# Kernel tuning notes

Hardware: AMD Instinct MI355X
Metric: run time of the kernel (lower is better)

Reference implementation:

```python
import jax, jax.numpy as jnp
import numpy as np

NUM_CLASSES = 4
NUM_PROTOTYPE = 8
D = 512
N = 200704  # 16 * 112 * 112 flattened tokens
GAMMA = 0.999        # EMA momentum (self.gamma)
EPS_SINK = 0.05      # sinkhorn epsilon
SINK_ITERS = 3       # sinkhorn iterations


def l2_normalize(x, axis=-1, eps=1e-12):
    n = jnp.linalg.norm(x, axis=axis, keepdims=True)
    return x / jnp.maximum(n, eps)


def layer_norm(x, g, b, eps=1e-5):
    mu = jnp.mean(x, axis=-1, keepdims=True)
    var = jnp.var(x, axis=-1, keepdims=True)
    return (x - mu) / jnp.sqrt(var + eps) * g + b


def masked_sinkhorn(scores, sel):
    # scores: [N, M] similarity to this class's prototypes; sel: [N] bool row mask
    # Faithful masked re-expression of distributed_sinkhorn (which gathers rows
    # where gt_seg == k); zeroed rows contribute nothing to any normalization.
    M = scores.shape[1]
    self32 = sel.astype(scores.dtype)[:, None]
    L = jnp.exp(scores / EPS_SINK) * self32           # [N, M]
    B = jnp.maximum(sel.sum(), 1).astype(scores.dtype)  # number of selected rows
    L = L / jnp.maximum(L.sum(), 1e-30)

    def body(L, _):
        col = L.sum(axis=0, keepdims=True)            # per-prototype mass
        L = L / jnp.maximum(col, 1e-30) / M
        row = L.sum(axis=1, keepdims=True)            # per-token mass
        L = (L / jnp.maximum(row, 1e-30) / B) * self32
        return L, None

    L, _ = jax.lax.scan(body, L, None, length=SINK_ITERS)
    L = L * B
    idx = jnp.argmax(L, axis=1)
    # hard one-hot assignment (deterministic stand-in for hard gumbel_softmax)
    q = jax.nn.one_hot(idx, M, dtype=scores.dtype) * self32
    return q


def prototype_learning(_c, pred, gt_seg, masks, protos, momentum):
    # _c [N, D], pred/gt_seg [N], masks [N, M, K], protos [K, M, D]
    correct = gt_seg == pred
    new_rows = []
    for k in range(NUM_CLASSES):  # small fixed class loop, as in the original
        sel = gt_seg == k
        q = masked_sinkhorn(masks[:, :, k], sel)      # [N, M]
        m_k = (correct & sel).astype(_c.dtype)        # [N]
        m_q = q * m_k[:, None]                        # masked assignments
        c_q = _c * m_k[:, None]                       # masked features
        f = m_q.T @ c_q                               # [M, D] aggregation
        n = m_q.sum(axis=0)                           # [M] per-prototype counts
        f = l2_normalize(f)
        upd = momentum * protos[k] + (1.0 - momentum) * f
        valid = (n != 0) & (sel.sum() > 0) & (n.sum() > 0)
        new_rows.append(jnp.where(valid[:, None], upd, protos[k]))
    return l2_normalize(jnp.stack(new_rows, axis=0))


def reference(feats, ln_gamma, ln_beta, mask_gamma, mask_beta, prototypes, gt_seg):
    _c = l2_normalize(layer_norm(feats, ln_gamma, ln_beta))       # [N, D]
    protos = l2_normalize(prototypes)                             # [K, M, D]
    masks = jnp.einsum('nd,kmd->nmk', _c, protos)                 # [N, M, K]
    out_seg = layer_norm(jnp.max(masks, axis=1), mask_gamma, mask_beta)  # [N, K]
    pred = jnp.argmax(out_seg, axis=1)
    new_protos = prototype_learning(_c, pred, gt_seg.astype(jnp.int32), masks, protos, GAMMA)
    return out_seg, new_protos


def setup_inputs() -> dict:
    key = jax.random.key(0)
    k1, k2, k3 = jax.random.split(key, 3)
    return {
        'feats': jax.random.normal(k1, (N, D), dtype=jnp.float32),
        'ln_gamma': jnp.ones((D,), jnp.float32),
        'ln_beta': jnp.zeros((D,), jnp.float32),
        'mask_gamma': jnp.ones((NUM_CLASSES,), jnp.float32),
        'mask_beta': jnp.zeros((NUM_CLASSES,), jnp.float32),
        'prototypes': 0.02 * jax.random.normal(k2, (NUM_CLASSES, NUM_PROTOTYPE, D), dtype=jnp.float32),
        'gt_seg': jax.random.randint(k3, (N,), 0, NUM_CLASSES, dtype=jnp.int32),
    }
```

## Files before the change

kernel.cpp:

```cpp
#include <hip/hip_runtime.h>
#include <math.h>

#define NROWS 200704
#define DIM 512
#define NKM 32

#define OFF_RED0   0
#define OFF_RED1   32
#define OFF_RED2   64
#define OFF_CNT    96
#define OFF_NP     100
#define OFF_CUR    192
#define OFF_BASE   2240
#define OFF_FACC   2304
#define ZERO_FLOATS 18688
#define OFF_SUMGP  18688
#define OFF_BP     18720
#define OFF_SCAL   18752
#define OFF_G2GB   18816
#define OFF_PROTON 19840
#define OFF_GPT    36224
#define OFF_RSTATS 52608
#define OFF_E      855424
#define OFF_FLAGS  2461056
#define OFF_SORT   2661760

__device__ __forceinline__ float block_reduce_sum(float v, float* sm) {
    int t = threadIdx.x;
    sm[t] = v; __syncthreads();
    #pragma unroll
    for (int o = 128; o > 0; o >>= 1) {
        if (t < o) sm[t] += sm[t + o];
        __syncthreads();
    }
    float r = sm[0]; __syncthreads();
    return r;
}

__global__ __launch_bounds__(256) void k_prep(const float* __restrict__ protos,
                                              const float* __restrict__ g,
                                              const float* __restrict__ b,
                                              float* __restrict__ ws) {
    __shared__ float sm[256];
    int t = threadIdx.x, j = blockIdx.x;
    if (j < NKM) {
        const float* p = protos + j * DIM;
        float v = p[t] * p[t] + p[t + 256] * p[t + 256];
        float ss = block_reduce_sum(v, sm);
        float den = fmaxf(sqrtf(ss), 1e-12f);
        float sgp = 0.f, sbp = 0.f;
        for (int d = t; d < DIM; d += 256) {
            float pn = p[d] / den;
            ws[OFF_PROTON + j * DIM + d] = pn;
            float gp = g[d] * pn;
            ws[OFF_GPT + j * DIM + d] = gp;
            sgp += gp; sbp += b[d] * pn;
        }
        float s1 = block_reduce_sum(sgp, sm);
        float s2 = block_reduce_sum(sbp, sm);
        if (t == 0) { ws[OFF_SUMGP + j] = s1; ws[OFF_BP + j] = s2; }
    } else {
        float a = 0.f, c = 0.f, e = 0.f;
        for (int d = t; d < DIM; d += 256) {
            float gv = g[d], bv = b[d];
            ws[OFF_G2GB + 2 * d]     = gv * gv;
            ws[OFF_G2GB + 2 * d + 1] = gv * bv;
            a += gv * gv; c += gv * bv; e += bv * bv;
        }
        float s1 = block_reduce_sum(a, sm);
        float s2 = block_reduce_sum(c, sm);
        float s3 = block_reduce_sum(e, sm);
        if (t == 0) { ws[OFF_SCAL] = s1; ws[OFF_SCAL + 1] = s2; ws[OFF_SCAL + 2] = s3; }
    }
}

#define STATS(XR, r) { \
    float _a = XR.x, _b = XR.y, _c = XR.z, _d = XR.w; \
    sx[r] += _a + _b + _c + _d; \
    float _a2 = _a * _a, _b2 = _b * _b, _c2 = _c * _c, _d2 = _d * _d; \
    sxx[r] += _a2 + _b2 + _c2 + _d2; \
    sxg2[r]  = fmaf(_a, gA.x, fmaf(_b, gA.z, fmaf(_c, gB.x, fmaf(_d, gB.z, sxg2[r])))); \
    sx2g2[r] = fmaf(_a2, gA.x, fmaf(_b2, gA.z, fmaf(_c2, gB.x, fmaf(_d2, gB.z, sx2g2[r])))); \
    sxgb[r]  = fmaf(_a, gA.y, fmaf(_b, gA.w, fmaf(_c, gB.y, fmaf(_d, gB.w, sxgb[r])))); \
}

#define EPILOGUE(DJ, r) { \
    float a_sx = sx[r], a_sxx = sxx[r], a_sxg2 = sxg2[r], a_sx2g2 = sx2g2[r], a_sxgb = sxgb[r]; \
    _Pragma("unroll") \
    for (int m = 1; m <= 4; m <<= 1) { \
        a_sx += __shfl_xor(a_sx, m, 64); \
        a_sxx += __shfl_xor(a_sxx, m, 64); \
        a_sxg2 += __shfl_xor(a_sxg2, m, 64); \
        a_sx2g2 += __shfl_xor(a_sx2g2, m, 64); \
        a_sxgb += __shfl_xor(a_sxgb, m, 64); \
        _Pragma("unroll") \
        for (int j = 0; j < NKM; ++j) DJ[j] += __shfl_xor(DJ[j], m, 64); \
    } \
    float mu = a_sx * (1.0f / DIM); \
    float var = a_sxx * (1.0f / DIM) - mu * mu; \
    float istd = 1.0f / sqrtf(var + 1e-5f); \
    float l2 = istd * istd * (a_sx2g2 - 2.0f * mu * a_sxg2 + mu * mu * s_scal[0]) \
             + 2.0f * istd * (a_sxgb - mu * s_scal[1]) + s_scal[2]; \
    float L = sqrtf(fmaxf(l2, 0.0f)); \
    float invL = 1.0f / fmaxf(L, 1e-12f); \
    float aa = istd * invL; \
    _Pragma("unroll") \
    for (int j = 0; j < NKM; ++j) DJ[j] = aa * (DJ[j] - mu * s_sumgp[j]) + invL * s_bp[j]; \
    float om[4]; \
    _Pragma("unroll") \
    for (int k = 0; k < 4; ++k) { \
        float m0 = DJ[k * 8]; \
        _Pragma("unroll") \
        for (int m = 1; m < 8; ++m) m0 = fmaxf(m0, DJ[k * 8 + m]); \
        om[k] = m0; \
    } \
    float mu4 = 0.25f * (om[0] + om[1] + om[2] + om[3]); \
    float e0 = om[0] - mu4, e1 = om[1] - mu4, e2 = om[2] - mu4, e3 = om[3] - mu4; \
    float v4 = 0.25f * (e0 * e0 + e1 * e1 + e2 * e2 + e3 * e3); \
    float is4 = 1.0f / sqrtf(v4 + 1e-5f); \
    float o0 = e0 * is4 * mg[0] + mb[0]; \
    float o1 = e1 * is4 * mg[1] + mb[1]; \
    float o2 = e2 * is4 * mg[2] + mb[2]; \
    float o3 = e3 * is4 * mg[3] + mb[3]; \
    int pred = 0; float bo = o0; \
    if (o1 > bo) { bo = o1; pred = 1; } \
    if (o2 > bo) { bo = o2; pred = 2; } \
    if (o3 > bo) { bo = o3; pred = 3; } \
    int row = row0 + r; \
    int gtv = gt_seg[row] & 3; \
    if (li == 0) { \
        *(float4*)(out + (size_t)row * 4) = make_float4(o0, o1, o2, o3); \
        ((int*)ws)[OFF_FLAGS + row] = gtv | ((pred == gtv) ? 4 : 0); \
        *(float4*)(ws + OFF_RSTATS + (size_t)row * 4) = make_float4(mu, istd, invL, 0.f); \
        float ev[8]; \
        _Pragma("unroll") \
        for (int m = 0; m < 8; ++m) { \
            float s = DJ[m]; \
            s = (gtv == 1) ? DJ[8 + m]  : s; \
            s = (gtv == 2) ? DJ[16 + m] : s; \
            s = (gtv == 3) ? DJ[24 + m] : s; \
            ev[m] = expf(s * 20.0f); \
        } \
        *(float4*)(ws + OFF_E + (size_t)row * 8)     = make_float4(ev[0], ev[1], ev[2], ev[3]); \
        *(float4*)(ws + OFF_E + (size_t)row * 8 + 4) = make_float4(ev[4], ev[5], ev[6], ev[7]); \
    } \
}

__global__ __launch_bounds__(256, 2) void k_main(const float* __restrict__ feats,
                                                 const float* __restrict__ mg,
                                                 const float* __restrict__ mb,
                                                 const int* __restrict__ gt_seg,
                                                 float* __restrict__ ws,
                                                 float* __restrict__ out) {
    __shared__ float gpt[NKM * DIM];
    __shared__ float s_sumgp[NKM], s_bp[NKM], s_scal[3];
    int t = threadIdx.x;
    {
        const float4* s4 = (const float4*)(ws + OFF_GPT);
        float4* d4 = (float4*)gpt;
        #pragma unroll 4
        for (int i = t; i < NKM * DIM / 4; i += 256) d4[i] = s4[i];
        if (t < NKM) { s_sumgp[t] = ws[OFF_SUMGP + t]; s_bp[t] = ws[OFF_BP + t]; }
        if (t < 3) s_scal[t] = ws[OFF_SCAL + t];
    }
    __syncthreads();
    int lane = t & 63, wv = t >> 6;
    int oct = lane >> 3, li = lane & 7;
    int row0 = blockIdx.x * 128 + wv * 32 + oct * 4;
    const float* xb = feats + (size_t)row0 * DIM;

    float dj0[NKM], dj1[NKM], dj2[NKM], dj3[NKM];
    #pragma unroll
    for (int j = 0; j < NKM; ++j) { dj0[j] = 0.f; dj1[j] = 0.f; dj2[j] = 0.f; dj3[j] = 0.f; }
    float sx[4] = {0,0,0,0}, sxx[4] = {0,0,0,0}, sxg2[4] = {0,0,0,0};
    float sx2g2[4] = {0,0,0,0}, sxgb[4] = {0,0,0,0};

    for (int c = 0; c < 16; ++c) {
        int d0 = c * 32 + li * 4;
        float4 x0 = *(const float4*)(xb + d0);
        float4 x1 = *(const float4*)(xb + DIM + d0);
        float4 x2 = *(const float4*)(xb + 2 * DIM + d0);
        float4 x3 = *(const float4*)(xb + 3 * DIM + d0);
        float4 gA = *(const float4*)(ws + OFF_G2GB + 2 * d0);
        float4 gB = *(const float4*)(ws + OFF_G2GB + 2 * d0 + 4);
        STATS(x0, 0) STATS(x1, 1) STATS(x2, 2) STATS(x3, 3)
        #pragma unroll
        for (int j = 0; j < NKM; ++j) {
            float4 w = *(const float4*)(gpt + j * DIM + d0);
            dj0[j] = fmaf(x0.x, w.x, fmaf(x0.y, w.y, fmaf(x0.z, w.z, fmaf(x0.w, w.w, dj0[j]))));
            dj1[j] = fmaf(x1.x, w.x, fmaf(x1.y, w.y, fmaf(x1.z, w.z, fmaf(x1.w, w.w, dj1[j]))));
            dj2[j] = fmaf(x2.x, w.x, fmaf(x2.y, w.y, fmaf(x2.z, w.z, fmaf(x2.w, w.w, dj2[j]))));
            dj3[j] = fmaf(x3.x, w.x, fmaf(x3.y, w.y, fmaf(x3.z, w.z, fmaf(x3.w, w.w, dj3[j]))));
        }
    }
    EPILOGUE(dj0, 0)
    EPILOGUE(dj1, 1)
    EPILOGUE(dj2, 2)
    EPILOGUE(dj3, 3)
}

__global__ __launch_bounds__(256) void k_red0(const int* __restrict__ gt_seg,
                                              float* __restrict__ ws) {
    __shared__ float lred[NKM];
    __shared__ int lcnt[4];
    int t = threadIdx.x;
    if (t < NKM) lred[t] = 0.f;
    if (t < 4) lcnt[t] = 0;
    __syncthreads();
    int row = blockIdx.x * 256 + t;
    int gt = gt_seg[row] & 3;
    float4 ea = *(const float4*)(ws + OFF_E + (size_t)row * 8);
    float4 eb = *(const float4*)(ws + OFF_E + (size_t)row * 8 + 4);
    atomicAdd(&lred[gt * 8 + 0], ea.x); atomicAdd(&lred[gt * 8 + 1], ea.y);
    atomicAdd(&lred[gt * 8 + 2], ea.z); atomicAdd(&lred[gt * 8 + 3], ea.w);
    atomicAdd(&lred[gt * 8 + 4], eb.x); atomicAdd(&lred[gt * 8 + 5], eb.y);
    atomicAdd(&lred[gt * 8 + 6], eb.z); atomicAdd(&lred[gt * 8 + 7], eb.w);
    atomicAdd(&lcnt[gt], 1);
    __syncthreads();
    if (t < NKM) atomicAdd(&ws[OFF_RED0 + t], lred[t]);
    if (t < 4) atomicAdd(&((int*)ws)[OFF_CNT + t], lcnt[t]);
}

__global__ __launch_bounds__(256) void k_red1(const int* __restrict__ gt_seg,
                                              float* __restrict__ ws) {
    __shared__ float S0p[4], Bk[4], a1[NKM], lred[NKM];
    int t = threadIdx.x;
    if (t < 4) {
        float s = 0.f;
        #pragma unroll
        for (int m = 0; m < 8; ++m) s += ws[OFF_RED0 + t * 8 + m];
        S0p[t] = fmaxf(s, 1e-30f);
        Bk[t] = fmaxf((float)((const int*)ws)[OFF_CNT + t], 1.0f);
    }
    if (t < NKM) lred[t] = 0.f;
    __syncthreads();
    if (t < NKM) {
        float col = ws[OFF_RED0 + t] / S0p[t >> 3];
        a1[t] = 1.0f / (fmaxf(col, 1e-30f) * 8.0f);
    }
    __syncthreads();
    int row = blockIdx.x * 256 + t;
    int gt = gt_seg[row] & 3;
    float4 ea = *(const float4*)(ws + OFF_E + (size_t)row * 8);
    float4 eb = *(const float4*)(ws + OFF_E + (size_t)row * 8 + 4);
    float ev[8] = {ea.x, ea.y, ea.z, ea.w, eb.x, eb.y, eb.z, eb.w};
    float dotv = 0.f;
    #pragma unroll
    for (int m = 0; m < 8; ++m) dotv += ev[m] * a1[gt * 8 + m];
    float row1 = dotv / S0p[gt];
    float r1 = 1.0f / (fmaxf(row1, 1e-30f) * Bk[gt]);
    #pragma unroll
    for (int m = 0; m < 8; ++m) atomicAdd(&lred[gt * 8 + m], ev[m] * r1);
    __syncthreads();
    if (t < NKM) atomicAdd(&ws[OFF_RED1 + t], lred[t]);
}

__global__ __launch_bounds__(256) void k_red2(const int* __restrict__ gt_seg,
                                              float* __restrict__ ws) {
    __shared__ float S0p[4], Bk[4], a1[NKM], a2[NKM], lred[NKM];
    int t = threadIdx.x;
    if (t < 4) {
        float s = 0.f;
        #pragma unroll
        for (int m = 0; m < 8; ++m) s += ws[OFF_RED0 + t * 8 + m];
        S0p[t] = fmaxf(s, 1e-30f);
        Bk[t] = fmaxf((float)((const int*)ws)[OFF_CNT + t], 1.0f);
    }
    if (t < NKM) lred[t] = 0.f;
    __syncthreads();
    if (t < NKM) {
        float col = ws[OFF_RED0 + t] / S0p[t >> 3];
        a1[t] = 1.0f / (fmaxf(col, 1e-30f) * 8.0f);
    }
    __syncthreads();
    if (t < NKM) {
        float col2 = a1[t] * ws[OFF_RED1 + t] / S0p[t >> 3];
        a2[t] = 1.0f / (fmaxf(col2, 1e-30f) * 8.0f);
    }
    __syncthreads();
    int row = blockIdx.x * 256 + t;
    int gt = gt_seg[row] & 3;
    float4 ea = *(const float4*)(ws + OFF_E + (size_t)row * 8);
    float4 eb = *(const float4*)(ws + OFF_E + (size_t)row * 8 + 4);
    float ev[8] = {ea.x, ea.y, ea.z, ea.w, eb.x, eb.y, eb.z, eb.w};
    float dotv = 0.f;
    #pragma unroll
    for (int m = 0; m < 8; ++m) dotv += ev[m] * a1[gt * 8 + m];
    float row1 = dotv / S0p[gt];
    float r1 = 1.0f / (fmaxf(row1, 1e-30f) * Bk[gt]);
    float dot2 = 0.f;
    #pragma unroll
    for (int m = 0; m < 8; ++m) dot2 += ev[m] * a1[gt * 8 + m] * a2[gt * 8 + m];
    float row2 = dot2 / S0p[gt] * r1;
    float r2 = 1.0f / (fmaxf(row2, 1e-30f) * Bk[gt]);
    #pragma unroll
    for (int m = 0; m < 8; ++m) atomicAdd(&lred[gt * 8 + m], ev[m] * r1 * r2);
    __syncthreads();
    if (t < NKM) atomicAdd(&ws[OFF_RED2 + t], lred[t]);
}

__global__ __launch_bounds__(256) void k_assign(float* __restrict__ ws) {
    __shared__ float S0p[4], Bk[4], a1[NKM], a2[NKM], F[NKM];
    __shared__ int ln[NKM];
    int t = threadIdx.x;
    if (t < 4) {
        float s = 0.f;
        #pragma unroll
        for (int m = 0; m < 8; ++m) s += ws[OFF_RED0 + t * 8 + m];
        S0p[t] = fmaxf(s, 1e-30f);
        Bk[t] = fmaxf((float)((const int*)ws)[OFF_CNT + t], 1.0f);
    }
    if (t < NKM) ln[t] = 0;
    __syncthreads();
    if (t < NKM) {
        float col = ws[OFF_RED0 + t] / S0p[t >> 3];
        a1[t] = 1.0f / (fmaxf(col, 1e-30f) * 8.0f);
    }
    __syncthreads();
    if (t < NKM) {
        float col2 = a1[t] * ws[OFF_RED1 + t] / S0p[t >> 3];
        a2[t] = 1.0f / (fmaxf(col2, 1e-30f) * 8.0f);
    }
    __syncthreads();
    if (t < NKM) {
        float col3 = a1[t] * a2[t] * ws[OFF_RED2 + t] / S0p[t >> 3];
        float a3 = 1.0f / (fmaxf(col3, 1e-30f) * 8.0f);
        F[t] = a1[t] * a2[t] * a3;
    }
    __syncthreads();
    int row = blockIdx.x * 256 + t;
    int flag = ((const int*)ws)[OFF_FLAGS + row];
    int slotv = -1;
    if (flag & 4) {
        int gt = flag & 3;
        float4 ea = *(const float4*)(ws + OFF_E + (size_t)row * 8);
        float4 eb = *(const float4*)(ws + OFF_E + (size_t)row * 8 + 4);
        float ev[8] = {ea.x, ea.y, ea.z, ea.w, eb.x, eb.y, eb.z, eb.w};
        int js = 0; float bv = ev[0] * F[gt * 8];
        #pragma unroll
        for (int m = 1; m < 8; ++m) {
            float v = ev[m] * F[gt * 8 + m];
            if (v > bv) { bv = v; js = m; }
        }
        slotv = gt * 8 + js;
        atomicAdd(&ln[slotv], 1);
    }
    ((int*)ws)[OFF_FLAGS + row] = slotv;
    __syncthreads();
    if (t < NKM && ln[t]) atomicAdd(&((int*)ws)[OFF_NP + t], ln[t]);
}

__global__ void k_prefix(float* __restrict__ ws) {
    if (threadIdx.x == 0) {
        int acc = 0;
        for (int s = 0; s < NKM; ++s) {
            ((int*)ws)[OFF_BASE + s] = acc;
            acc += ((const int*)ws)[OFF_NP + s];
        }
    }
}

__global__ __launch_bounds__(256) void k_scatter(float* __restrict__ ws) {
    int row = blockIdx.x * 256 + threadIdx.x;
    int s = ((const int*)ws)[OFF_FLAGS + row];
    if (s >= 0) {
        int pos = atomicAdd(&((int*)ws)[OFF_CUR + s * 64], 1);
        ((int*)ws)[OFF_SORT + ((const int*)ws)[OFF_BASE + s] + pos] = row;
    }
}

__global__ __launch_bounds__(256) void k_agg(const float* __restrict__ feats,
                                             const float* __restrict__ g,
                                             const float* __restrict__ b,
                                             float* __restrict__ ws) {
    int t = threadIdx.x;
    int slot = blockIdx.x >> 4, ch = blockIdx.x & 15;
    int n = ((const int*)ws)[OFF_NP + slot];
    int base = ((const int*)ws)[OFF_BASE + slot];
    int r0 = base + (ch * n) / 16;
    int r1 = base + ((ch + 1) * n) / 16;
    if (r0 >= r1) return;
    const int* sortl = (const int*)ws + OFF_SORT;
    float2 gv = *(const float2*)(g + 2 * t);
    float2 bv = *(const float2*)(b + 2 * t);
    float acc0 = 0.f, acc1 = 0.f;
    #pragma unroll 4
    for (int i = r0; i < r1; ++i) {
        int row = sortl[i];
        float4 rs = *(const float4*)(ws + OFF_RSTATS + (size_t)row * 4);
        float2 x = *(const float2*)(feats + (size_t)row * DIM + 2 * t);
        acc0 += ((x.x - rs.x) * rs.y * gv.x + bv.x) * rs.z;
        acc1 += ((x.y - rs.x) * rs.y * gv.y + bv.y) * rs.z;
    }
    atomicAdd(&ws[OFF_FACC + slot * DIM + 2 * t],     acc0);
    atomicAdd(&ws[OFF_FACC + slot * DIM + 2 * t + 1], acc1);
}

__global__ __launch_bounds__(256) void k_final(float* __restrict__ ws,
                                               float* __restrict__ out) {
    __shared__ float sm[256];
    int t = threadIdx.x, j = blockIdx.x, k = j >> 3;
    int nj = ((const int*)ws)[OFF_NP + j];
    int ck = ((const int*)ws)[OFF_CNT + k];
    int nsum = 0;
    #pragma unroll
    for (int m = 0; m < 8; ++m) nsum += ((const int*)ws)[OFF_NP + k * 8 + m];
    int d0 = t, d1 = t + 256;
    float f0 = ws[OFF_FACC + j * DIM + d0];
    float f1 = ws[OFF_FACC + j * DIM + d1];
    float nf = block_reduce_sum(f0 * f0 + f1 * f1, sm);
    float fin = 1.0f / fmaxf(sqrtf(nf), 1e-12f);
    float pn0 = ws[OFF_PROTON + j * DIM + d0];
    float pn1 = ws[OFF_PROTON + j * DIM + d1];
    bool valid = (nj != 0) && (ck > 0) && (nsum > 0);
    float r0 = valid ? (0.999f * pn0 + 0.001f * (f0 * fin)) : pn0;
    float r1 = valid ? (0.999f * pn1 + 0.001f * (f1 * fin)) : pn1;
    float n2 = block_reduce_sum(r0 * r0 + r1 * r1, sm);
    float i2 = 1.0f / fmaxf(sqrtf(n2), 1e-12f);
    out[(size_t)NROWS * 4 + j * DIM + d0] = r0 * i2;
    out[(size_t)NROWS * 4 + j * DIM + d1] = r1 * i2;
}

extern "C" void kernel_launch(void* const* d_in, const int* in_sizes, int n_in,
                              void* d_out, int out_size, void* d_ws, size_t ws_size,
                              hipStream_t stream) {
    const float* feats = (const float*)d_in[0];
    const float* ln_g  = (const float*)d_in[1];
    const float* ln_b  = (const float*)d_in[2];
    const float* mg    = (const float*)d_in[3];
    const float* mb    = (const float*)d_in[4];
    const float* prot  = (const float*)d_in[5];
    const int*   gt    = (const int*)d_in[6];
    float* out = (float*)d_out;
    float* ws  = (float*)d_ws;

    hipMemsetAsync(d_ws, 0, ZERO_FLOATS * 4, stream);
    k_prep<<<33, 256, 0, stream>>>(prot, ln_g, ln_b, ws);
    k_main<<<NROWS / 128, 256, 0, stream>>>(feats, mg, mb, gt, ws, out);
    k_red0<<<NROWS / 256, 256, 0, stream>>>(gt, ws);
    k_red1<<<NROWS / 256, 256, 0, stream>>>(gt, ws);
    k_red2<<<NROWS / 256, 256, 0, stream>>>(gt, ws);
    k_assign<<<NROWS / 256, 256, 0, stream>>>(ws);
    k_prefix<<<1, 64, 0, stream>>>(ws);
    k_scatter<<<NROWS / 256, 256, 0, stream>>>(ws);
    k_agg<<<NKM * 16, 256, 0, stream>>>(feats, ln_g, ln_b, ws);
    k_final<<<NKM, 256, 0, stream>>>(ws, out);
}
```

Before: 804.3 us.

## Compute token-prototype similarities with split-bf16 MFMA instead of scalar FP32 FMAs

```diff
diff --git a/kernel.cpp b/kernel.cpp
--- a/kernel.cpp
+++ b/kernel.cpp
@@ -1,4 +1,5 @@
 #include <hip/hip_runtime.h>
+#include <hip/hip_bf16.h>
 #include <math.h>
 
 #define NROWS 200704
@@ -19,11 +20,24 @@
 #define OFF_SCAL   18752
 #define OFF_G2GB   18816
 #define OFF_PROTON 19840
-#define OFF_GPT    36224
-#define OFF_RSTATS 52608
-#define OFF_E      855424
-#define OFF_FLAGS  2461056
-#define OFF_SORT   2661760
+#define OFF_WHI    36224
+#define OFF_WLO    44544
+#define OFF_RSTATS 52864
+#define OFF_E      855680
+#define OFF_FLAGS  2461312
+#define OFF_SORT   2662016
+
+typedef __attribute__((ext_vector_type(8)))  short short8;
+typedef __attribute__((ext_vector_type(16))) float f32x16;
+
+union ABFrag { unsigned int u[4]; short8 s; };
+
+__device__ __forceinline__ unsigned int pk2(float a, float b) {
+    __hip_bfloat162 h2 = __float22bfloat162_rn(make_float2(a, b));
+    union { __hip_bfloat162 h; unsigned int u; } cv;
+    cv.h = h2;
+    return cv.u;
+}
 
 __device__ __forceinline__ float block_reduce_sum(float v, float* sm) {
     int t = threadIdx.x;
@@ -49,12 +63,18 @@
         float ss = block_reduce_sum(v, sm);
         float den = fmaxf(sqrtf(ss), 1e-12f);
         float sgp = 0.f, sbp = 0.f;
+        unsigned short* whi = (unsigned short*)ws + 2 * OFF_WHI + j * 520;
+        unsigned short* wlo = (unsigned short*)ws + 2 * OFF_WLO + j * 520;
         for (int d = t; d < DIM; d += 256) {
             float pn = p[d] / den;
             ws[OFF_PROTON + j * DIM + d] = pn;
-            float gp = g[d] * pn;
-            ws[OFF_GPT + j * DIM + d] = gp;
-            sgp += gp; sbp += b[d] * pn;
+            float w = g[d] * pn;
+            unsigned int hb = pk2(w, 0.f) & 0xffffu;
+            float hf = __uint_as_float(hb << 16);
+            unsigned int lb = pk2(w - hf, 0.f) & 0xffffu;
+            whi[d] = (unsigned short)hb;
+            wlo[d] = (unsigned short)lb;
+            sgp += w; sbp += b[d] * pn;
         }
         float s1 = block_reduce_sum(sgp, sm);
         float s2 = block_reduce_sum(sbp, sm);
@@ -74,77 +94,17 @@
     }
 }
 
-#define STATS(XR, r) { \
-    float _a = XR.x, _b = XR.y, _c = XR.z, _d = XR.w; \
-    sx[r] += _a + _b + _c + _d; \
-    float _a2 = _a * _a, _b2 = _b * _b, _c2 = _c * _c, _d2 = _d * _d; \
-    sxx[r] += _a2 + _b2 + _c2 + _d2; \
-    sxg2[r]  = fmaf(_a, gA.x, fmaf(_b, gA.z, fmaf(_c, gB.x, fmaf(_d, gB.z, sxg2[r])))); \
-    sx2g2[r] = fmaf(_a2, gA.x, fmaf(_b2, gA.z, fmaf(_c2, gB.x, fmaf(_d2, gB.z, sx2g2[r])))); \
-    sxgb[r]  = fmaf(_a, gA.y, fmaf(_b, gA.w, fmaf(_c, gB.y, fmaf(_d, gB.w, sxgb[r])))); \
-}
-
-#define EPILOGUE(DJ, r) { \
-    float a_sx = sx[r], a_sxx = sxx[r], a_sxg2 = sxg2[r], a_sx2g2 = sx2g2[r], a_sxgb = sxgb[r]; \
-    _Pragma("unroll") \
-    for (int m = 1; m <= 4; m <<= 1) { \
-        a_sx += __shfl_xor(a_sx, m, 64); \
-        a_sxx += __shfl_xor(a_sxx, m, 64); \
-        a_sxg2 += __shfl_xor(a_sxg2, m, 64); \
-        a_sx2g2 += __shfl_xor(a_sx2g2, m, 64); \
-        a_sxgb += __shfl_xor(a_sxgb, m, 64); \
-        _Pragma("unroll") \
-        for (int j = 0; j < NKM; ++j) DJ[j] += __shfl_xor(DJ[j], m, 64); \
-    } \
-    float mu = a_sx * (1.0f / DIM); \
-    float var = a_sxx * (1.0f / DIM) - mu * mu; \
-    float istd = 1.0f / sqrtf(var + 1e-5f); \
-    float l2 = istd * istd * (a_sx2g2 - 2.0f * mu * a_sxg2 + mu * mu * s_scal[0]) \
-             + 2.0f * istd * (a_sxgb - mu * s_scal[1]) + s_scal[2]; \
-    float L = sqrtf(fmaxf(l2, 0.0f)); \
-    float invL = 1.0f / fmaxf(L, 1e-12f); \
-    float aa = istd * invL; \
-    _Pragma("unroll") \
-    for (int j = 0; j < NKM; ++j) DJ[j] = aa * (DJ[j] - mu * s_sumgp[j]) + invL * s_bp[j]; \
-    float om[4]; \
-    _Pragma("unroll") \
-    for (int k = 0; k < 4; ++k) { \
-        float m0 = DJ[k * 8]; \
-        _Pragma("unroll") \
-        for (int m = 1; m < 8; ++m) m0 = fmaxf(m0, DJ[k * 8 + m]); \
-        om[k] = m0; \
-    } \
-    float mu4 = 0.25f * (om[0] + om[1] + om[2] + om[3]); \
-    float e0 = om[0] - mu4, e1 = om[1] - mu4, e2 = om[2] - mu4, e3 = om[3] - mu4; \
-    float v4 = 0.25f * (e0 * e0 + e1 * e1 + e2 * e2 + e3 * e3); \
-    float is4 = 1.0f / sqrtf(v4 + 1e-5f); \
-    float o0 = e0 * is4 * mg[0] + mb[0]; \
-    float o1 = e1 * is4 * mg[1] + mb[1]; \
-    float o2 = e2 * is4 * mg[2] + mb[2]; \
-    float o3 = e3 * is4 * mg[3] + mb[3]; \
-    int pred = 0; float bo = o0; \
-    if (o1 > bo) { bo = o1; pred = 1; } \
-    if (o2 > bo) { bo = o2; pred = 2; } \
-    if (o3 > bo) { bo = o3; pred = 3; } \
-    int row = row0 + r; \
-    int gtv = gt_seg[row] & 3; \
-    if (li == 0) { \
-        *(float4*)(out + (size_t)row * 4) = make_float4(o0, o1, o2, o3); \
-        ((int*)ws)[OFF_FLAGS + row] = gtv | ((pred == gtv) ? 4 : 0); \
-        *(float4*)(ws + OFF_RSTATS + (size_t)row * 4) = make_float4(mu, istd, invL, 0.f); \
-        float ev[8]; \
-        _Pragma("unroll") \
-        for (int m = 0; m < 8; ++m) { \
-            float s = DJ[m]; \
-            s = (gtv == 1) ? DJ[8 + m]  : s; \
-            s = (gtv == 2) ? DJ[16 + m] : s; \
-            s = (gtv == 3) ? DJ[24 + m] : s; \
-            ev[m] = expf(s * 20.0f); \
-        } \
-        *(float4*)(ws + OFF_E + (size_t)row * 8)     = make_float4(ev[0], ev[1], ev[2], ev[3]); \
-        *(float4*)(ws + OFF_E + (size_t)row * 8 + 4) = make_float4(ev[4], ev[5], ev[6], ev[7]); \
-    } \
-}
+#define ST1(XV, G2V, GBV) { float _x = (XV); float _x2 = _x * _x; \
+    sx += _x; sxx += _x2; \
+    sxg2  = fmaf(_x,  (G2V), sxg2); \
+    sx2g2 = fmaf(_x2, (G2V), sx2g2); \
+    sxgb  = fmaf(_x,  (GBV), sxgb); }
+
+#define PAIRSPLIT(A0, B0, HO, LO) { \
+    unsigned int _h = pk2((A0), (B0)); HO = _h; \
+    float _ha = __uint_as_float(_h << 16); \
+    float _hb = __uint_as_float(_h & 0xffff0000u); \
+    LO = pk2((A0) - _ha, (B0) - _hb); }
 
 __global__ __launch_bounds__(256, 2) void k_main(const float* __restrict__ feats,
                                                  const float* __restrict__ mg,
@@ -152,51 +112,126 @@
                                                  const int* __restrict__ gt_seg,
                                                  float* __restrict__ ws,
                                                  float* __restrict__ out) {
-    __shared__ float gpt[NKM * DIM];
-    __shared__ float s_sumgp[NKM], s_bp[NKM], s_scal[3];
+    __shared__ __align__(16) unsigned short ls_whi[32 * 520];
+    __shared__ __align__(16) unsigned short ls_wlo[32 * 520];
+    __shared__ __align__(16) float ls_g2gb[1024];
     int t = threadIdx.x;
     {
-        const float4* s4 = (const float4*)(ws + OFF_GPT);
-        float4* d4 = (float4*)gpt;
-        #pragma unroll 4
-        for (int i = t; i < NKM * DIM / 4; i += 256) d4[i] = s4[i];
-        if (t < NKM) { s_sumgp[t] = ws[OFF_SUMGP + t]; s_bp[t] = ws[OFF_BP + t]; }
-        if (t < 3) s_scal[t] = ws[OFF_SCAL + t];
-    }
-    __syncthreads();
-    int lane = t & 63, wv = t >> 6;
-    int oct = lane >> 3, li = lane & 7;
-    int row0 = blockIdx.x * 128 + wv * 32 + oct * 4;
-    const float* xb = feats + (size_t)row0 * DIM;
-
-    float dj0[NKM], dj1[NKM], dj2[NKM], dj3[NKM];
-    #pragma unroll
-    for (int j = 0; j < NKM; ++j) { dj0[j] = 0.f; dj1[j] = 0.f; dj2[j] = 0.f; dj3[j] = 0.f; }
-    float sx[4] = {0,0,0,0}, sxx[4] = {0,0,0,0}, sxg2[4] = {0,0,0,0};
-    float sx2g2[4] = {0,0,0,0}, sxgb[4] = {0,0,0,0};
-
-    for (int c = 0; c < 16; ++c) {
-        int d0 = c * 32 + li * 4;
-        float4 x0 = *(const float4*)(xb + d0);
-        float4 x1 = *(const float4*)(xb + DIM + d0);
-        float4 x2 = *(const float4*)(xb + 2 * DIM + d0);
-        float4 x3 = *(const float4*)(xb + 3 * DIM + d0);
-        float4 gA = *(const float4*)(ws + OFF_G2GB + 2 * d0);
-        float4 gB = *(const float4*)(ws + OFF_G2GB + 2 * d0 + 4);
-        STATS(x0, 0) STATS(x1, 1) STATS(x2, 2) STATS(x3, 3)
-        #pragma unroll
-        for (int j = 0; j < NKM; ++j) {
-            float4 w = *(const float4*)(gpt + j * DIM + d0);
-            dj0[j] = fmaf(x0.x, w.x, fmaf(x0.y, w.y, fmaf(x0.z, w.z, fmaf(x0.w, w.w, dj0[j]))));
-            dj1[j] = fmaf(x1.x, w.x, fmaf(x1.y, w.y, fmaf(x1.z, w.z, fmaf(x1.w, w.w, dj1[j]))));
-            dj2[j] = fmaf(x2.x, w.x, fmaf(x2.y, w.y, fmaf(x2.z, w.z, fmaf(x2.w, w.w, dj2[j]))));
-            dj3[j] = fmaf(x3.x, w.x, fmaf(x3.y, w.y, fmaf(x3.z, w.z, fmaf(x3.w, w.w, dj3[j]))));
-        }
-    }
-    EPILOGUE(dj0, 0)
-    EPILOGUE(dj1, 1)
-    EPILOGUE(dj2, 2)
-    EPILOGUE(dj3, 3)
+        const float4* sh = (const float4*)(ws + OFF_WHI);
+        float4* dh = (float4*)ls_whi;
+        for (int i = t; i < 2080; i += 256) dh[i] = sh[i];
+        const float4* sl = (const float4*)(ws + OFF_WLO);
+        float4* dl = (float4*)ls_wlo;
+        for (int i = t; i < 2080; i += 256) dl[i] = sl[i];
+        const float4* sg = (const float4*)(ws + OFF_G2GB);
+        float4* dg = (float4*)ls_g2gb;
+        dg[t] = sg[t];
+    }
+    __syncthreads();
+
+    int wv = t >> 6, l = t & 63;
+    int h = l >> 5, c32 = l & 31;
+    int row0 = blockIdx.x * 128 + wv * 32;
+    const float* xrow = feats + (size_t)(row0 + c32) * DIM + h * 8;
+    const unsigned short* bhp = ls_whi + c32 * 520 + h * 8;
+    const unsigned short* blp = ls_wlo + c32 * 520 + h * 8;
+    const float4* g4 = ((const float4*)ls_g2gb) + h * 4;
+
+    f32x16 acc;
+    #pragma unroll
+    for (int i = 0; i < 16; ++i) acc[i] = 0.f;
+    float sx = 0.f, sxx = 0.f, sxg2 = 0.f, sx2g2 = 0.f, sxgb = 0.f;
+
+    #pragma unroll 4
+    for (int kc = 0; kc < 32; ++kc) {
+        float4 xa = *(const float4*)(xrow + kc * 16);
+        float4 xb = *(const float4*)(xrow + kc * 16 + 4);
+        float4 ga  = g4[kc * 8 + 0];
+        float4 gb_ = g4[kc * 8 + 1];
+        float4 gc  = g4[kc * 8 + 2];
+        float4 gd  = g4[kc * 8 + 3];
+        ST1(xa.x, ga.x,  ga.y)  ST1(xa.y, ga.z,  ga.w)
+        ST1(xa.z, gb_.x, gb_.y) ST1(xa.w, gb_.z, gb_.w)
+        ST1(xb.x, gc.x,  gc.y)  ST1(xb.y, gc.z,  gc.w)
+        ST1(xb.z, gd.x,  gd.y)  ST1(xb.w, gd.z,  gd.w)
+        ABFrag ah, al;
+        PAIRSPLIT(xa.x, xa.y, ah.u[0], al.u[0])
+        PAIRSPLIT(xa.z, xa.w, ah.u[1], al.u[1])
+        PAIRSPLIT(xb.x, xb.y, ah.u[2], al.u[2])
+        PAIRSPLIT(xb.z, xb.w, ah.u[3], al.u[3])
+        short8 bh = *(const short8*)(bhp + kc * 16);
+        short8 bl = *(const short8*)(blp + kc * 16);
+        acc = __builtin_amdgcn_mfma_f32_32x32x16_bf16(ah.s, bh, acc, 0, 0, 0);
+        acc = __builtin_amdgcn_mfma_f32_32x32x16_bf16(ah.s, bl, acc, 0, 0, 0);
+        acc = __builtin_amdgcn_mfma_f32_32x32x16_bf16(al.s, bh, acc, 0, 0, 0);
+    }
+
+    sx    += __shfl_xor(sx, 32, 64);
+    sxx   += __shfl_xor(sxx, 32, 64);
+    sxg2  += __shfl_xor(sxg2, 32, 64);
+    sx2g2 += __shfl_xor(sx2g2, 32, 64);
+    sxgb  += __shfl_xor(sxgb, 32, 64);
+
+    float scal0 = ws[OFF_SCAL], scal1 = ws[OFF_SCAL + 1], scal2 = ws[OFF_SCAL + 2];
+    float mu  = sx * (1.0f / DIM);
+    float var = sxx * (1.0f / DIM) - mu * mu;
+    float istd = 1.0f / sqrtf(var + 1e-5f);
+    float l2v = istd * istd * (sx2g2 - 2.0f * mu * sxg2 + mu * mu * scal0)
+              + 2.0f * istd * (sxgb - mu * scal1) + scal2;
+    float L = sqrtf(fmaxf(l2v, 0.0f));
+    float invL = 1.0f / fmaxf(L, 1e-12f);
+    float aa = istd * invL;
+    if (l < 32)
+        *(float4*)(ws + OFF_RSTATS + (size_t)(row0 + l) * 4) = make_float4(mu, istd, invL, 0.f);
+
+    float wsum = ws[OFF_SUMGP + c32], wbp = ws[OFF_BP + c32];
+    float mg0 = mg[0], mg1 = mg[1], mg2 = mg[2], mg3 = mg[3];
+    float mb0 = mb[0], mb1 = mb[1], mb2 = mb[2], mb3 = mb[3];
+    int q = c32 >> 3;
+    int li8 = c32 & 7;
+
+    #pragma unroll
+    for (int r = 0; r < 16; ++r) {
+        int rowt = (r & 3) + 8 * (r >> 2) + 4 * h;
+        int grow = row0 + rowt;
+        float mu_r = __shfl(mu, rowt, 64);
+        float aa_r = __shfl(aa, rowt, 64);
+        float il_r = __shfl(invL, rowt, 64);
+        float s = aa_r * (acc[r] - mu_r * wsum) + il_r * wbp;
+        float m = s;
+        m = fmaxf(m, __shfl_xor(m, 1, 64));
+        m = fmaxf(m, __shfl_xor(m, 2, 64));
+        m = fmaxf(m, __shfl_xor(m, 4, 64));
+        float vA = m;
+        float vB = __shfl_xor(vA, 8, 64);
+        float vC = __shfl_xor(vA, 16, 64);
+        float vD = __shfl_xor(vB, 16, 64);
+        float o0 = (q == 0) ? vA : (q == 1) ? vB : (q == 2) ? vC : vD;
+        float o1 = (q == 1) ? vA : (q == 0) ? vB : (q == 3) ? vC : vD;
+        float o2 = (q == 2) ? vA : (q == 3) ? vB : (q == 0) ? vC : vD;
+        float o3 = (q == 3) ? vA : (q == 2) ? vB : (q == 1) ? vC : vD;
+        float mu4 = 0.25f * (o0 + o1 + o2 + o3);
+        float e0 = o0 - mu4, e1 = o1 - mu4, e2 = o2 - mu4, e3 = o3 - mu4;
+        float v4 = 0.25f * (e0 * e0 + e1 * e1 + e2 * e2 + e3 * e3);
+        float is4 = 1.0f / sqrtf(v4 + 1e-5f);
+        float f0 = e0 * is4 * mg0 + mb0;
+        float f1 = e1 * is4 * mg1 + mb1;
+        float f2 = e2 * is4 * mg2 + mb2;
+        float f3 = e3 * is4 * mg3 + mb3;
+        int pred = 0; float bo = f0;
+        if (f1 > bo) { bo = f1; pred = 1; }
+        if (f2 > bo) { bo = f2; pred = 2; }
+        if (f3 > bo) { bo = f3; pred = 3; }
+        int gtv = gt_seg[grow] & 3;
+        if (c32 == 0) {
+            *(float4*)(out + (size_t)grow * 4) = make_float4(f0, f1, f2, f3);
+            ((int*)ws)[OFF_FLAGS + grow] = gtv | ((pred == gtv) ? 4 : 0);
+        }
+        if (q == gtv) {
+            float ev = expf(s * 20.0f);
+            ws[OFF_E + (size_t)grow * 8 + li8] = ev;
+        }
+    }
 }
 
 __global__ __launch_bounds__(256) void k_red0(const int* __restrict__ gt_seg,
```

Result: faster. 699.2 us (-13.1%).
